# Optimization experiments

Hardware: AMD Instinct MI355X
Metric: run time of the kernel (lower is better)

Reference implementation:

```python
import jax, jax.numpy as jnp
import numpy as np

N = 50000   # nodes per node type
D = 128     # in/out channels
E = 500000  # edges per edge type


def setup_inputs() -> dict:
    key = jax.random.key(0)
    ks = jax.random.split(key, 24)
    s = 1.0 / np.sqrt(D)
    def w(k, shape):
        return jax.random.normal(k, shape, jnp.float32) * s
    inp = {
        "x_a": jax.random.normal(ks[0], (N, D), jnp.float32),
        "x_b": jax.random.normal(ks[1], (N, D), jnp.float32),
        "edge_e1": jax.random.randint(ks[2], (2, E), 0, N),  # a -> b
        "edge_e2": jax.random.randint(ks[3], (2, E), 0, N),  # b -> a
        "edge_e3": jax.random.randint(ks[4], (2, E), 0, N),  # b -> a
    }
    i = 5
    for e in ("e1", "e2", "e3"):
        inp[f"Ws_{e}"] = w(ks[i], (D, D)); i += 1
        inp[f"Wt_{e}"] = w(ks[i], (D, D)); i += 1
        inp[f"wih_{e}"] = w(ks[i], (3 * D, D)); i += 1
        inp[f"whh_{e}"] = w(ks[i], (3 * D, D)); i += 1
        inp[f"bih_{e}"] = jnp.zeros((3 * D,), jnp.float32)
        inp[f"bhh_{e}"] = jnp.zeros((3 * D,), jnp.float32)
    return inp


def _gru_cell(x, h, wih, whh, bih, bhh):
    # PyTorch nn.GRUCell semantics: x = input, h = hidden
    gi = x @ wih.T + bih
    gh = h @ whh.T + bhh
    ir, iz, inn = jnp.split(gi, 3, axis=1)
    hr, hz, hn = jnp.split(gh, 3, axis=1)
    r = jax.nn.sigmoid(ir + hr)
    z = jax.nn.sigmoid(iz + hz)
    n = jnp.tanh(inn + r * hn)
    return (1.0 - z) * n + z * h


def _edge_type(x_src, x_tgt, edge, Ws, Wt, wih, whh, bih, bhh):
    sx = x_src @ Ws.T                       # [Ns, D] per-edge-type source linear (no bias)
    tx = x_tgt @ Wt.T                       # [Nt, D] per-edge-type target linear
    msg = sx[edge[0]]                       # [E, D]  gather by source index
    agg = jax.ops.segment_sum(msg, edge[1], num_segments=x_tgt.shape[0])  # scatter-sum
    return _gru_cell(tx, agg, wih, whh, bih, bhh)


def reference(x_a, x_b, edge_e1, edge_e2, edge_e3,
              Ws_e1, Wt_e1, wih_e1, whh_e1, bih_e1, bhh_e1,
              Ws_e2, Wt_e2, wih_e2, whh_e2, bih_e2, bhh_e2,
              Ws_e3, Wt_e3, wih_e3, whh_e3, bih_e3, bhh_e3):
    # edge type e1: a -> b  (div['b'] = 1)
    out_b = _edge_type(x_a, x_b, edge_e1, Ws_e1, Wt_e1, wih_e1, whh_e1, bih_e1, bhh_e1)
    # edge types e2, e3: b -> a  (div['a'] = 2)
    out_a = _edge_type(x_b, x_a, edge_e2, Ws_e2, Wt_e2, wih_e2, whh_e2, bih_e2, bhh_e2)
    out_a = out_a + _edge_type(x_b, x_a, edge_e3, Ws_e3, Wt_e3, wih_e3, whh_e3, bih_e3, bhh_e3)
    out_a = out_a / 2.0
    out_a = jax.nn.relu(out_a)
    out_b = jax.nn.relu(out_b)
    return jnp.stack([out_a, out_b])  # [2, N, D]
```

## Files before the change

### kernel.cpp

```cpp
#include <hip/hip_runtime.h>
#include <hip/hip_bf16.h>
#include <stdint.h>
#include <math.h>

#define NN 50000
#define DD 128
#define EE 500000
#define ROWT 1563
#define NBIN 98
#define CHB 245

typedef __attribute__((ext_vector_type(8))) short bfx8;
typedef __attribute__((ext_vector_type(4))) short bfx4;
typedef __attribute__((ext_vector_type(4))) float f32x4;
typedef __attribute__((ext_vector_type(4))) int i32x4;
typedef unsigned short u16;

static __device__ __forceinline__ short f2bf(float f) {
  union { float f; uint32_t u; } v; v.f = f;
  uint32_t r = (v.u + 0x7fffu + ((v.u >> 16) & 1u)) >> 16;
  return (short)r;
}
static __device__ __forceinline__ float bf2f(short b) {
  union { uint32_t u; float f; } v; v.u = ((uint32_t)(uint16_t)b) << 16;
  return v.f;
}

static __device__ __forceinline__ void gl_lds16(const short* g, short* l) {
  __builtin_amdgcn_global_load_lds(
      (const __attribute__((address_space(1))) unsigned int*)g,
      (__attribute__((address_space(3))) unsigned int*)l, 16, 0, 0);
}

static __device__ __forceinline__ bfx8 load_pk(const short* p, int ct, int ks, int lane) {
  return *reinterpret_cast<const bfx8*>(p + ((((size_t)ct * 4 + ks) * 64 + lane) << 3));
}

struct PrepArgs {
  const float* csrc[2]; short* cdst[2];
  const float* A[6]; const float* B[6]; short* pout[6];
  const float* psrc[3]; short* pdst[3];
  const int* edge[3]; int* ccnt;
};

__global__ __launch_bounds__(256) void k_prep(PrepArgs p) {
  const int y = blockIdx.y;
  if (y < 2) {
    int i = (blockIdx.x * 256 + threadIdx.x) * 4;
    if (i >= NN * DD) return;
    f32x4 v = *reinterpret_cast<const f32x4*>(p.csrc[y] + i);
    bfx4 o;
    o[0]=f2bf(v[0]); o[1]=f2bf(v[1]); o[2]=f2bf(v[2]); o[3]=f2bf(v[3]);
    *reinterpret_cast<bfx4*>(p.cdst[y] + i) = o;
  } else if (y < 8) {
    if (blockIdx.x >= 192) return;
    const int e = y - 2;
    const float* A = p.A[e];
    const float* B = p.B[e];
    int tid = blockIdx.x * 256 + threadIdx.x;
    int i = tid >> 7, j = tid & 127;
    float acc = 0.f;
    #pragma unroll 4
    for (int k = 0; k < 128; ++k) acc += A[i * 128 + k] * B[k * 128 + j];
    int ct = i >> 4;
    int lane = (i & 15) | ((((j & 31) >> 3)) << 4);
    int ks = j >> 5;
    int elem = j & 7;
    p.pout[e][(((size_t)(ct * 4 + ks) * 64 + lane) << 3) + elem] = f2bf(acc);
  } else if (y < 11) {
    if (blockIdx.x >= 8) return;
    const int jb = y - 8;
    int tid = blockIdx.x * 256 + threadIdx.x;
    int lane = tid & 63, ks = (tid >> 6) & 3, ct = tid >> 8;
    const float* s = p.psrc[jb] + (size_t)(ct * 16 + (lane & 15)) * 128 + ks * 32 + ((lane >> 4) << 3);
    bfx8 o;
    #pragma unroll
    for (int i = 0; i < 8; ++i) o[i] = f2bf(s[i]);
    *reinterpret_cast<bfx8*>(p.pdst[jb] + ((size_t)tid << 3)) = o;
  } else {
    if (blockIdx.x >= CHB) return;
    const int t = y - 11, tid = threadIdx.x;
    __shared__ int cnt[NBIN];
    for (int b = tid; b < NBIN; b += 256) cnt[b] = 0;
    __syncthreads();
    const int* ed = p.edge[t];
    int base = blockIdx.x * 2048;
    #pragma unroll
    for (int m = 0; m < 8; ++m) {
      int i = base + m * 256 + tid;
      if (i < EE) atomicAdd(&cnt[ed[EE + i] >> 9], 1);
    }
    __syncthreads();
    for (int b = tid; b < NBIN; b += 256)
      if (cnt[b]) atomicAdd(&p.ccnt[t * NBIN + b], cnt[b]);
  }
}

struct CsrArgs {
  const int* edge[3];
  int* ccnt;
  int* cstart;
  int* ccur;
  uint32_t* cbkt[3];
  int* offs[3];
  u16* bucket[3];
};

__global__ __launch_bounds__(384) void k_cscan(CsrArgs a) {
  __shared__ int buf[3][128];
  int ty = threadIdx.x >> 7;
  int i = threadIdx.x & 127;
  int v = (i < NBIN) ? a.ccnt[ty * NBIN + i] : 0;
  buf[ty][i] = v;
  __syncthreads();
  for (int off = 1; off < 128; off <<= 1) {
    int tv = (i >= off) ? buf[ty][i - off] : 0;
    __syncthreads();
    buf[ty][i] += tv;
    __syncthreads();
  }
  if (i < NBIN) {
    int excl = buf[ty][i] - v;
    a.cstart[ty * NBIN + i] = excl;
    a.ccur[ty * NBIN + i] = excl;
  }
}

__global__ __launch_bounds__(256) void k_cbin(CsrArgs a) {
  const int t = blockIdx.y, tid = threadIdx.x;
  __shared__ int cnt[NBIN], cur[NBIN];
  for (int b = tid; b < NBIN; b += 256) cnt[b] = 0;
  __syncthreads();
  const int* ed = a.edge[t];
  int base = blockIdx.x * 4096;
  #pragma unroll
  for (int m = 0; m < 16; ++m) {
    int i = base + m * 256 + tid;
    if (i < EE) atomicAdd(&cnt[ed[EE + i] >> 9], 1);
  }
  __syncthreads();
  for (int b = tid; b < NBIN; b += 256)
    cur[b] = cnt[b] ? atomicAdd(&a.ccur[t * NBIN + b], cnt[b]) : 0;
  __syncthreads();
  uint32_t* cb = a.cbkt[t];
  #pragma unroll
  for (int m = 0; m < 16; ++m) {
    int i = base + m * 256 + tid;
    if (i < EE) {
      int tg = ed[EE + i];
      int b = tg >> 9;
      int pos = atomicAdd(&cur[b], 1);
      cb[pos] = (uint32_t)ed[i] | ((uint32_t)(tg & 511) << 20);
    }
  }
}

__global__ __launch_bounds__(256) void k_fsort(CsrArgs a) {
  const int t = blockIdx.y, bin = blockIdx.x, tid = threadIdx.x;
  __shared__ int rc[512], rcur[512], sb[256];
  int s0 = a.cstart[t * NBIN + bin];
  int cntb = a.ccnt[t * NBIN + bin];
  rc[tid] = 0; rc[tid + 256] = 0;
  __syncthreads();
  const uint32_t* cb = a.cbkt[t];
  for (int i = tid; i < cntb; i += 256) atomicAdd(&rc[cb[s0 + i] >> 20], 1);
  __syncthreads();
  int A = rc[2 * tid], B = rc[2 * tid + 1], s = A + B;
  sb[tid] = s;
  __syncthreads();
  for (int off = 1; off < 256; off <<= 1) {
    int v = (tid >= off) ? sb[tid - off] : 0;
    __syncthreads();
    sb[tid] += v;
    __syncthreads();
  }
  int excl = sb[tid] - s;
  rcur[2 * tid] = s0 + excl;
  rcur[2 * tid + 1] = s0 + excl + A;
  int rows0 = bin << 9;
  int nr = NN - rows0; if (nr > 512) nr = 512;
  if (2 * tid < nr)     a.offs[t][rows0 + 2 * tid]     = s0 + excl + A;
  if (2 * tid + 1 < nr) a.offs[t][rows0 + 2 * tid + 1] = s0 + excl + A + B;
  __syncthreads();
  u16* fb = a.bucket[t];
  for (int i = tid; i < cntb; i += 256) {
    uint32_t e = cb[s0 + i];
    int pos = atomicAdd(&rcur[e >> 20], 1);
    fb[pos] = (u16)e;
  }
}

struct GArgs {
  const int* offs[3]; const u16* bkt[3];
  const short* xsrc[3]; short* agg[3];
};

__global__ __launch_bounds__(256) void k_gather(GArgs a) {
  const int ty = blockIdx.y;
  const int* __restrict__ offs = a.offs[ty];
  const u16* __restrict__ bucket = a.bkt[ty];
  const short* __restrict__ xsrc = a.xsrc[ty];
  short* __restrict__ agg = a.agg[ty];
  int tid = threadIdx.x;
  int row = blockIdx.x * 32 + (tid >> 3);
  if (row >= NN) return;
  int c0 = (tid & 7) * 16;
  int start = row ? offs[row - 1] : 0;
  int end = offs[row];
  f32x4 s0 = (f32x4)(0.f), s1 = (f32x4)(0.f), s2 = (f32x4)(0.f), s3 = (f32x4)(0.f);
  int i = start;
  for (; i + 8 <= end; i += 8) {
    const short* pp[8];
    #pragma unroll
    for (int m = 0; m < 8; ++m) pp[m] = xsrc + (size_t)bucket[i + m] * DD + c0;
    #pragma unroll
    for (int m = 0; m < 8; ++m) {
      bfx8 u = *reinterpret_cast<const bfx8*>(pp[m]);
      bfx8 v = *reinterpret_cast<const bfx8*>(pp[m] + 8);
      #pragma unroll
      for (int j = 0; j < 4; ++j) {
        s0[j] += bf2f(u[j]); s1[j] += bf2f(u[4+j]);
        s2[j] += bf2f(v[j]); s3[j] += bf2f(v[4+j]);
      }
    }
  }
  for (; i + 4 <= end; i += 4) {
    const short* pp[4];
    #pragma unroll
    for (int m = 0; m < 4; ++m) pp[m] = xsrc + (size_t)bucket[i + m] * DD + c0;
    #pragma unroll
    for (int m = 0; m < 4; ++m) {
      bfx8 u = *reinterpret_cast<const bfx8*>(pp[m]);
      bfx8 v = *reinterpret_cast<const bfx8*>(pp[m] + 8);
      #pragma unroll
      for (int j = 0; j < 4; ++j) {
        s0[j] += bf2f(u[j]); s1[j] += bf2f(u[4+j]);
        s2[j] += bf2f(v[j]); s3[j] += bf2f(v[4+j]);
      }
    }
  }
  for (; i < end; ++i) {
    const short* p = xsrc + (size_t)bucket[i] * DD + c0;
    bfx8 u = *reinterpret_cast<const bfx8*>(p), v = *reinterpret_cast<const bfx8*>(p + 8);
    #pragma unroll
    for (int j = 0; j < 4; ++j) {
      s0[j] += bf2f(u[j]); s1[j] += bf2f(u[4+j]);
      s2[j] += bf2f(v[j]); s3[j] += bf2f(v[4+j]);
    }
  }
  short* d = agg + (size_t)row * DD + c0;
  bfx8 o0, o1;
  #pragma unroll
  for (int j = 0; j < 4; ++j) {
    o0[j] = f2bf(s0[j]); o0[4+j] = f2bf(s1[j]);
    o1[j] = f2bf(s2[j]); o1[4+j] = f2bf(s3[j]);
  }
  *reinterpret_cast<bfx8*>(d) = o0;
  *reinterpret_cast<bfx8*>(d + 8) = o1;
}

static __device__ __forceinline__ void gru8(const f32x4 h[2], const f32x4 ai[2][3],
                                            const f32x4 ah[2][3],
                                            float bir, float biz, float bin,
                                            float bhr, float bhz, float bhn,
                                            f32x4 res[2]) {
  #pragma unroll
  for (int rf = 0; rf < 2; ++rf)
    #pragma unroll
    for (int q = 0; q < 4; ++q) {
      float ir = ai[rf][0][q] + bir, iz = ai[rf][1][q] + biz, in = ai[rf][2][q] + bin;
      float hr = ah[rf][0][q] + bhr, hz = ah[rf][1][q] + bhz, hn = ah[rf][2][q] + bhn;
      float rr = 1.f / (1.f + __expf(-(ir + hr)));
      float zz = 1.f / (1.f + __expf(-(iz + hz)));
      float t2 = in + rr * hn;
      float nn = 1.f - 2.f / (__expf(2.f * t2) + 1.f);
      res[rf][q] = (1.f - zz) * nn + zz * h[rf][q];
    }
}

static __device__ __forceinline__ void gru_unit(
    const short* lds, int gbase, int ctw, int lane,
    const short* wsp, const short* combp, const short* whhsp,
    f32x4 (&h)[2], f32x4 (&ai)[2][3], f32x4 (&ah)[2][3]) {
  #pragma unroll
  for (int rf = 0; rf < 2; ++rf) {
    h[rf] = (f32x4)(0.f);
    #pragma unroll
    for (int g = 0; g < 3; ++g) { ai[rf][g] = (f32x4)(0.f); ah[rf][g] = (f32x4)(0.f); }
  }
  #pragma unroll
  for (int ks = 0; ks < 4; ++ks) {
    bfx8 x0 = *reinterpret_cast<const bfx8*>(lds + (0 + ks) * 512 + lane * 8);
    bfx8 x1 = *reinterpret_cast<const bfx8*>(lds + (4 + ks) * 512 + lane * 8);
    bfx8 g0 = *reinterpret_cast<const bfx8*>(lds + (gbase + ks) * 512 + lane * 8);
    bfx8 g1 = *reinterpret_cast<const bfx8*>(lds + (gbase + 4 + ks) * 512 + lane * 8);
    bfx8 bws = load_pk(wsp, ctw, ks, lane);
    h[0] = __builtin_amdgcn_mfma_f32_16x16x32_bf16(g0, bws, h[0], 0, 0, 0);
    h[1] = __builtin_amdgcn_mfma_f32_16x16x32_bf16(g1, bws, h[1], 0, 0, 0);
    #pragma unroll
    for (int g = 0; g < 3; ++g) {
      int ct = g * 8 + ctw;
      bfx8 bi = load_pk(combp, ct, ks, lane);
      bfx8 bh = load_pk(whhsp, ct, ks, lane);
      ai[0][g] = __builtin_amdgcn_mfma_f32_16x16x32_bf16(x0, bi, ai[0][g], 0, 0, 0);
      ai[1][g] = __builtin_amdgcn_mfma_f32_16x16x32_bf16(x1, bi, ai[1][g], 0, 0, 0);
      ah[0][g] = __builtin_amdgcn_mfma_f32_16x16x32_bf16(g0, bh, ah[0][g], 0, 0, 0);
      ah[1][g] = __builtin_amdgcn_mfma_f32_16x16x32_bf16(g1, bh, ah[1][g], 0, 0, 0);
    }
  }
}

struct GG1Args {
  const short* aggX; const short* xt;
  const short* wsp; const short* combp; const short* whhsp;
  const float* bih; const float* bhh;
  float* out;
};

__global__ __launch_bounds__(512) void k_ggru1(GG1Args a) {
  __shared__ short lds[16 * 512];
  const int wave = threadIdx.x >> 6, lane = threadIdx.x & 63;
  const int rbase = blockIdx.x * 32;
  const int ctw = wave;

  #pragma unroll
  for (int i = 0; i < 2; ++i) {
    int f = wave * 2 + i;
    const short* src = (f & 8) ? a.aggX : a.xt;
    int r = rbase + ((f >> 2) & 1) * 16 + (lane & 15);
    if (r >= NN) r = NN - 1;
    gl_lds16(src + (size_t)r * DD + (f & 3) * 32 + ((lane >> 4) << 3), lds + f * 512);
  }
  __syncthreads();

  f32x4 h[2], ai[2][3], ah[2][3];
  gru_unit(lds, 8, ctw, lane, a.wsp, a.combp, a.whhsp, h, ai, ah);

  const int col = ctw * 16 + (lane & 15);
  f32x4 res[2];
  gru8(h, ai, ah, a.bih[col], a.bih[128 + col], a.bih[256 + col],
       a.bhh[col], a.bhh[128 + col], a.bhh[256 + col], res);
  const int lq = (lane >> 4) << 2;
  #pragma unroll
  for (int rf = 0; rf < 2; ++rf)
    #pragma unroll
    for (int q = 0; q < 4; ++q) {
      int r = rbase + rf * 16 + lq + q;
      if (r < NN) a.out[(size_t)r * DD + col] = fmaxf(res[rf][q], 0.f);
    }
}

struct GG2Args {
  const short* agg2; const short* agg3; const short* xt;
  const short* wsp2; const short* combp2; const short* whhsp2;
  const short* wsp3; const short* combp3; const short* whhsp3;
  const float* bih2; const float* bhh2;
  const float* bih3; const float* bhh3;
  float* out;
};

__global__ __launch_bounds__(512) void k_ggru2(GG2Args a) {
  __shared__ short lds[24 * 512];
  float* r3buf = (float*)lds;
  const int wave = threadIdx.x >> 6, lane = threadIdx.x & 63;
  const int rbase = (blockIdx.x >> 1) * 32;
  const int colblk = blockIdx.x & 1;
  const int unit = wave >> 2;
  const int ctw = colblk * 4 + (wave & 3);

  #pragma unroll
  for (int i = 0; i < 3; ++i) {
    int f = wave * 3 + i;
    const short* src = (f < 8) ? a.xt : ((f < 16) ? a.agg2 : a.agg3);
    int r = rbase + ((f >> 2) & 1) * 16 + (lane & 15);
    if (r >= NN) r = NN - 1;
    gl_lds16(src + (size_t)r * DD + (f & 3) * 32 + ((lane >> 4) << 3), lds + f * 512);
  }
  __syncthreads();

  const short* wspU   = unit ? a.wsp3   : a.wsp2;
  const short* combpU = unit ? a.combp3 : a.combp2;
  const short* whhspU = unit ? a.whhsp3 : a.whhsp2;
  const float* bihU   = unit ? a.bih3   : a.bih2;
  const float* bhhU   = unit ? a.bhh3   : a.bhh2;
  const int gbase = unit ? 16 : 8;

  f32x4 h[2], ai[2][3], ah[2][3];
  gru_unit(lds, gbase, ctw, lane, wspU, combpU, whhspU, h, ai, ah);

  const int col = ctw * 16 + (lane & 15);
  const int cl = (wave & 3) * 16 + (lane & 15);
  const int lq = (lane >> 4) << 2;
  f32x4 res[2];
  gru8(h, ai, ah, bihU[col], bihU[128 + col], bihU[256 + col],
       bhhU[col], bhhU[128 + col], bhhU[256 + col], res);

  __syncthreads();
  if (unit == 1) {
    #pragma unroll
    for (int rf = 0; rf < 2; ++rf)
      #pragma unroll
      for (int q = 0; q < 4; ++q)
        r3buf[(rf * 16 + lq + q) * 68 + cl] = res[rf][q];
  }
  __syncthreads();
  if (unit == 0) {
    #pragma unroll
    for (int rf = 0; rf < 2; ++rf)
      #pragma unroll
      for (int q = 0; q < 4; ++q) {
        int r = rbase + rf * 16 + lq + q;
        if (r < NN) {
          float r3 = r3buf[(rf * 16 + lq + q) * 68 + cl];
          a.out[(size_t)r * DD + col] = fmaxf((res[rf][q] + r3) * 0.5f, 0.f);
        }
      }
  }
}

extern "C" void kernel_launch(void* const* d_in, const int* in_sizes, int n_in,
                              void* d_out, int out_size, void* d_ws, size_t ws_size,
                              hipStream_t stream) {
  const float* x_a = (const float*)d_in[0];
  const float* x_b = (const float*)d_in[1];
  const int* edges[3] = {(const int*)d_in[2], (const int*)d_in[3], (const int*)d_in[4]};
  const float *Ws[3], *Wt[3], *wih[3], *whh[3], *bih[3], *bhh[3];
  for (int e = 0; e < 3; ++e) {
    int b = 5 + e * 6;
    Ws[e]  = (const float*)d_in[b + 0];
    Wt[e]  = (const float*)d_in[b + 1];
    wih[e] = (const float*)d_in[b + 2];
    whh[e] = (const float*)d_in[b + 3];
    bih[e] = (const float*)d_in[b + 4];
    bhh[e] = (const float*)d_in[b + 5];
  }

  char* ws = (char*)d_ws;
  short* xa_bf  = (short*)ws;
  short* xb_bf  = (short*)(ws + 12800000);
  short* aggX   = (short*)(ws + 25600000);
  int*   offs   = (int*)(ws + 64000000);
  u16*   bucket = (u16*)(ws + 64600000);
  uint32_t* cbkt= (uint32_t*)(ws + 67600000);
  short* pk     = (short*)(ws + 73600000);
  int*   ccnt   = (int*)(ws + 74300000);
  int*   cstart = (int*)(ws + 74310000);
  int*   ccur   = (int*)(ws + 74320000);
  short *wsp[3], *combp[3], *whhsp[3];
  short* aggp[3];
  int* offsp[3]; u16* bktp[3]; uint32_t* cbktp[3];
  for (int e = 0; e < 3; ++e) {
    short* base = pk + (size_t)e * 114688;
    wsp[e] = base; combp[e] = base + 16384; whhsp[e] = base + 65536;
    aggp[e]  = aggX + (size_t)e * NN * DD;
    offsp[e] = offs + (size_t)e * 50000;
    bktp[e]  = bucket + (size_t)e * 500000;
    cbktp[e] = cbkt + (size_t)e * 500000;
  }

  (void)hipMemsetAsync(ccnt, 0, 3 * NBIN * sizeof(int), stream);

  PrepArgs pa;
  pa.csrc[0] = x_a; pa.cdst[0] = xa_bf;
  pa.csrc[1] = x_b; pa.cdst[1] = xb_bf;
  for (int e = 0; e < 3; ++e) {
    pa.A[e] = wih[e];     pa.B[e] = Wt[e]; pa.pout[e] = combp[e];
    pa.A[3 + e] = whh[e]; pa.B[3 + e] = Ws[e]; pa.pout[3 + e] = whhsp[e];
    pa.psrc[e] = Ws[e];   pa.pdst[e] = wsp[e];
    pa.edge[e] = edges[e];
  }
  pa.ccnt = ccnt;
  hipLaunchKernelGGL(k_prep, dim3(6250, 14), dim3(256), 0, stream, pa);

  CsrArgs ca;
  for (int e = 0; e < 3; ++e) {
    ca.edge[e] = edges[e];
    ca.cbkt[e] = cbktp[e];
    ca.offs[e] = offsp[e];
    ca.bucket[e] = bktp[e];
  }
  ca.ccnt = ccnt; ca.cstart = cstart; ca.ccur = ccur;
  hipLaunchKernelGGL(k_cscan, dim3(1), dim3(384), 0, stream, ca);
  hipLaunchKernelGGL(k_cbin, dim3((EE + 4095) / 4096, 3), dim3(256), 0, stream, ca);
  hipLaunchKernelGGL(k_fsort, dim3(NBIN, 3), dim3(256), 0, stream, ca);

  GArgs ga;
  const short* srcb[3] = {xa_bf, xb_bf, xb_bf};
  for (int e = 0; e < 3; ++e) {
    ga.offs[e] = offsp[e]; ga.bkt[e] = bktp[e];
    ga.xsrc[e] = srcb[e];  ga.agg[e] = aggp[e];
  }
  hipLaunchKernelGGL(k_gather, dim3(ROWT, 3), dim3(256), 0, stream, ga);

  float* out_a = (float*)d_out;
  float* out_b = (float*)d_out + (size_t)NN * DD;

  GG1Args g1 = {aggp[0], xb_bf, wsp[0], combp[0], whhsp[0], bih[0], bhh[0], out_b};
  hipLaunchKernelGGL(k_ggru1, dim3(ROWT), dim3(512), 0, stream, g1);

  GG2Args g2 = {aggp[1], aggp[2], xa_bf,
                wsp[1], combp[1], whhsp[1],
                wsp[2], combp[2], whhsp[2],
                bih[1], bhh[1], bih[2], bhh[2], out_a};
  hipLaunchKernelGGL(k_ggru2, dim3(ROWT * 2), dim3(512), 0, stream, g2);
}
```

Before: 228.7 us.

## Fuse CSR gather into GRU kernels, writing aggregates straight to LDS

```diff
diff --git a/kernel.cpp b/kernel.cpp
--- a/kernel.cpp
+++ b/kernel.cpp
@@ -190,73 +190,43 @@
   }
 }
 
-struct GArgs {
-  const int* offs[3]; const u16* bkt[3];
-  const short* xsrc[3]; short* agg[3];
-};
-
-__global__ __launch_bounds__(256) void k_gather(GArgs a) {
-  const int ty = blockIdx.y;
-  const int* __restrict__ offs = a.offs[ty];
-  const u16* __restrict__ bucket = a.bkt[ty];
-  const short* __restrict__ xsrc = a.xsrc[ty];
-  short* __restrict__ agg = a.agg[ty];
-  int tid = threadIdx.x;
-  int row = blockIdx.x * 32 + (tid >> 3);
-  if (row >= NN) return;
-  int c0 = (tid & 7) * 16;
-  int start = row ? offs[row - 1] : 0;
-  int end = offs[row];
-  f32x4 s0 = (f32x4)(0.f), s1 = (f32x4)(0.f), s2 = (f32x4)(0.f), s3 = (f32x4)(0.f);
-  int i = start;
-  for (; i + 8 <= end; i += 8) {
-    const short* pp[8];
-    #pragma unroll
-    for (int m = 0; m < 8; ++m) pp[m] = xsrc + (size_t)bucket[i + m] * DD + c0;
-    #pragma unroll
-    for (int m = 0; m < 8; ++m) {
-      bfx8 u = *reinterpret_cast<const bfx8*>(pp[m]);
-      bfx8 v = *reinterpret_cast<const bfx8*>(pp[m] + 8);
+static __device__ __forceinline__ void gather_slice(
+    const int* __restrict__ offs, const u16* __restrict__ bucket,
+    const short* __restrict__ xsrc, short* lds, int gbase,
+    int rbase, int lr, int c0) {
+  int row = rbase + lr;
+  f32x4 sa = (f32x4)(0.f), sb = (f32x4)(0.f);
+  if (row < NN) {
+    int start = row ? offs[row - 1] : 0;
+    int end = offs[row];
+    int i = start;
+    for (; i + 4 <= end; i += 4) {
+      const short* p0 = xsrc + (size_t)bucket[i]     * DD + c0;
+      const short* p1 = xsrc + (size_t)bucket[i + 1] * DD + c0;
+      const short* p2 = xsrc + (size_t)bucket[i + 2] * DD + c0;
+      const short* p3 = xsrc + (size_t)bucket[i + 3] * DD + c0;
+      bfx8 u0 = *reinterpret_cast<const bfx8*>(p0);
+      bfx8 u1 = *reinterpret_cast<const bfx8*>(p1);
+      bfx8 u2 = *reinterpret_cast<const bfx8*>(p2);
+      bfx8 u3 = *reinterpret_cast<const bfx8*>(p3);
       #pragma unroll
       for (int j = 0; j < 4; ++j) {
-        s0[j] += bf2f(u[j]); s1[j] += bf2f(u[4+j]);
-        s2[j] += bf2f(v[j]); s3[j] += bf2f(v[4+j]);
+        sa[j] += bf2f(u0[j]) + bf2f(u1[j]) + bf2f(u2[j]) + bf2f(u3[j]);
+        sb[j] += bf2f(u0[4+j]) + bf2f(u1[4+j]) + bf2f(u2[4+j]) + bf2f(u3[4+j]);
       }
     }
-  }
-  for (; i + 4 <= end; i += 4) {
-    const short* pp[4];
-    #pragma unroll
-    for (int m = 0; m < 4; ++m) pp[m] = xsrc + (size_t)bucket[i + m] * DD + c0;
-    #pragma unroll
-    for (int m = 0; m < 4; ++m) {
-      bfx8 u = *reinterpret_cast<const bfx8*>(pp[m]);
-      bfx8 v = *reinterpret_cast<const bfx8*>(pp[m] + 8);
+    for (; i < end; ++i) {
+      bfx8 u = *reinterpret_cast<const bfx8*>(xsrc + (size_t)bucket[i] * DD + c0);
       #pragma unroll
-      for (int j = 0; j < 4; ++j) {
-        s0[j] += bf2f(u[j]); s1[j] += bf2f(u[4+j]);
-        s2[j] += bf2f(v[j]); s3[j] += bf2f(v[4+j]);
-      }
-    }
-  }
-  for (; i < end; ++i) {
-    const short* p = xsrc + (size_t)bucket[i] * DD + c0;
-    bfx8 u = *reinterpret_cast<const bfx8*>(p), v = *reinterpret_cast<const bfx8*>(p + 8);
-    #pragma unroll
-    for (int j = 0; j < 4; ++j) {
-      s0[j] += bf2f(u[j]); s1[j] += bf2f(u[4+j]);
-      s2[j] += bf2f(v[j]); s3[j] += bf2f(v[4+j]);
-    }
-  }
-  short* d = agg + (size_t)row * DD + c0;
-  bfx8 o0, o1;
-  #pragma unroll
-  for (int j = 0; j < 4; ++j) {
-    o0[j] = f2bf(s0[j]); o0[4+j] = f2bf(s1[j]);
-    o1[j] = f2bf(s2[j]); o1[4+j] = f2bf(s3[j]);
-  }
-  *reinterpret_cast<bfx8*>(d) = o0;
-  *reinterpret_cast<bfx8*>(d + 8) = o1;
+      for (int j = 0; j < 4; ++j) { sa[j] += bf2f(u[j]); sb[j] += bf2f(u[4+j]); }
+    }
+  }
+  int f = gbase + ((lr >> 4) << 2) + (c0 >> 5);
+  int ln = (lr & 15) | (((c0 & 31) >> 3) << 4);
+  bfx8 o;
+  #pragma unroll
+  for (int j = 0; j < 4; ++j) { o[j] = f2bf(sa[j]); o[4+j] = f2bf(sb[j]); }
+  *reinterpret_cast<bfx8*>(lds + f * 512 + ln * 8) = o;
 }
 
 static __device__ __forceinline__ void gru8(const f32x4 h[2], const f32x4 ai[2][3],
@@ -311,32 +281,34 @@
 }
 
 struct GG1Args {
-  const short* aggX; const short* xt;
+  const short* xgat;
+  const short* xt;
+  const int* offs; const u16* bucket;
   const short* wsp; const short* combp; const short* whhsp;
   const float* bih; const float* bhh;
   float* out;
 };
 
-__global__ __launch_bounds__(512) void k_ggru1(GG1Args a) {
+__global__ __launch_bounds__(512) void k_ggru1f(GG1Args a) {
   __shared__ short lds[16 * 512];
   const int wave = threadIdx.x >> 6, lane = threadIdx.x & 63;
   const int rbase = blockIdx.x * 32;
-  const int ctw = wave;
-
-  #pragma unroll
-  for (int i = 0; i < 2; ++i) {
-    int f = wave * 2 + i;
-    const short* src = (f & 8) ? a.aggX : a.xt;
-    int r = rbase + ((f >> 2) & 1) * 16 + (lane & 15);
+
+  {
+    int r = rbase + ((wave >> 2) & 1) * 16 + (lane & 15);
     if (r >= NN) r = NN - 1;
-    gl_lds16(src + (size_t)r * DD + (f & 3) * 32 + ((lane >> 4) << 3), lds + f * 512);
+    gl_lds16(a.xt + (size_t)r * DD + (wave & 3) * 32 + ((lane >> 4) << 3), lds + wave * 512);
+  }
+  {
+    int t = threadIdx.x;
+    gather_slice(a.offs, a.bucket, a.xgat, lds, 8, rbase, t >> 4, (t & 15) * 8);
   }
   __syncthreads();
 
   f32x4 h[2], ai[2][3], ah[2][3];
-  gru_unit(lds, 8, ctw, lane, a.wsp, a.combp, a.whhsp, h, ai, ah);
-
-  const int col = ctw * 16 + (lane & 15);
+  gru_unit(lds, 8, wave, lane, a.wsp, a.combp, a.whhsp, h, ai, ah);
+
+  const int col = wave * 16 + (lane & 15);
   f32x4 res[2];
   gru8(h, ai, ah, a.bih[col], a.bih[128 + col], a.bih[256 + col],
        a.bhh[col], a.bhh[128 + col], a.bhh[256 + col], res);
@@ -351,7 +323,10 @@
 }
 
 struct GG2Args {
-  const short* agg2; const short* agg3; const short* xt;
+  const short* xgat;
+  const short* xt;
+  const int* offs2; const u16* bucket2;
+  const int* offs3; const u16* bucket3;
   const short* wsp2; const short* combp2; const short* whhsp2;
   const short* wsp3; const short* combp3; const short* whhsp3;
   const float* bih2; const float* bhh2;
@@ -359,22 +334,26 @@
   float* out;
 };
 
-__global__ __launch_bounds__(512) void k_ggru2(GG2Args a) {
+__global__ __launch_bounds__(1024) void k_ggru2f(GG2Args a) {
   __shared__ short lds[24 * 512];
-  float* r3buf = (float*)lds;
+  float* r3buf = (float*)(lds + 8 * 512);
   const int wave = threadIdx.x >> 6, lane = threadIdx.x & 63;
-  const int rbase = (blockIdx.x >> 1) * 32;
-  const int colblk = blockIdx.x & 1;
-  const int unit = wave >> 2;
-  const int ctw = colblk * 4 + (wave & 3);
-
-  #pragma unroll
-  for (int i = 0; i < 3; ++i) {
-    int f = wave * 3 + i;
-    const short* src = (f < 8) ? a.xt : ((f < 16) ? a.agg2 : a.agg3);
-    int r = rbase + ((f >> 2) & 1) * 16 + (lane & 15);
+  const int rbase = blockIdx.x * 32;
+  const int unit = wave >> 3;
+  const int ctw = wave & 7;
+
+  if (unit == 0) {
+    int r = rbase + ((wave >> 2) & 1) * 16 + (lane & 15);
     if (r >= NN) r = NN - 1;
-    gl_lds16(src + (size_t)r * DD + (f & 3) * 32 + ((lane >> 4) << 3), lds + f * 512);
+    gl_lds16(a.xt + (size_t)r * DD + (wave & 3) * 32 + ((lane >> 4) << 3), lds + wave * 512);
+  }
+  {
+    int t = threadIdx.x;
+    int ty = t >> 9;
+    int lr = (t >> 4) & 31;
+    int c0 = (t & 15) * 8;
+    gather_slice(ty ? a.offs3 : a.offs2, ty ? a.bucket3 : a.bucket2,
+                 a.xgat, lds, 8 + ty * 8, rbase, lr, c0);
   }
   __syncthreads();
 
@@ -383,13 +362,11 @@
   const short* whhspU = unit ? a.whhsp3 : a.whhsp2;
   const float* bihU   = unit ? a.bih3   : a.bih2;
   const float* bhhU   = unit ? a.bhh3   : a.bhh2;
-  const int gbase = unit ? 16 : 8;
 
   f32x4 h[2], ai[2][3], ah[2][3];
-  gru_unit(lds, gbase, ctw, lane, wspU, combpU, whhspU, h, ai, ah);
+  gru_unit(lds, unit ? 16 : 8, ctw, lane, wspU, combpU, whhspU, h, ai, ah);
 
   const int col = ctw * 16 + (lane & 15);
-  const int cl = (wave & 3) * 16 + (lane & 15);
   const int lq = (lane >> 4) << 2;
   f32x4 res[2];
   gru8(h, ai, ah, bihU[col], bihU[128 + col], bihU[256 + col],
@@ -401,7 +378,7 @@
     for (int rf = 0; rf < 2; ++rf)
       #pragma unroll
       for (int q = 0; q < 4; ++q)
-        r3buf[(rf * 16 + lq + q) * 68 + cl] = res[rf][q];
+        r3buf[(rf * 16 + lq + q) * 128 + col] = res[rf][q];
   }
   __syncthreads();
   if (unit == 0) {
@@ -411,7 +388,7 @@
       for (int q = 0; q < 4; ++q) {
         int r = rbase + rf * 16 + lq + q;
         if (r < NN) {
-          float r3 = r3buf[(rf * 16 + lq + q) * 68 + cl];
+          float r3 = r3buf[(rf * 16 + lq + q) * 128 + col];
           a.out[(size_t)r * DD + col] = fmaxf((res[rf][q] + r3) * 0.5f, 0.f);
         }
       }
@@ -438,21 +415,18 @@
   char* ws = (char*)d_ws;
   short* xa_bf  = (short*)ws;
   short* xb_bf  = (short*)(ws + 12800000);
-  short* aggX   = (short*)(ws + 25600000);
-  int*   offs   = (int*)(ws + 64000000);
-  u16*   bucket = (u16*)(ws + 64600000);
-  uint32_t* cbkt= (uint32_t*)(ws + 67600000);
-  short* pk     = (short*)(ws + 73600000);
-  int*   ccnt   = (int*)(ws + 74300000);
-  int*   cstart = (int*)(ws + 74310000);
-  int*   ccur   = (int*)(ws + 74320000);
+  int*   offs   = (int*)(ws + 25600000);
+  u16*   bucket = (u16*)(ws + 26200000);
+  uint32_t* cbkt= (uint32_t*)(ws + 29200000);
+  short* pk     = (short*)(ws + 35200000);
+  int*   ccnt   = (int*)(ws + 35900000);
+  int*   cstart = (int*)(ws + 35910000);
+  int*   ccur   = (int*)(ws + 35920000);
   short *wsp[3], *combp[3], *whhsp[3];
-  short* aggp[3];
   int* offsp[3]; u16* bktp[3]; uint32_t* cbktp[3];
   for (int e = 0; e < 3; ++e) {
     short* base = pk + (size_t)e * 114688;
     wsp[e] = base; combp[e] = base + 16384; whhsp[e] = base + 65536;
-    aggp[e]  = aggX + (size_t)e * NN * DD;
     offsp[e] = offs + (size_t)e * 50000;
     bktp[e]  = bucket + (size_t)e * 500000;
     cbktp[e] = cbkt + (size_t)e * 500000;
@@ -484,23 +458,25 @@
   hipLaunchKernelGGL(k_cbin, dim3((EE + 4095) / 4096, 3), dim3(256), 0, stream, ca);
   hipLaunchKernelGGL(k_fsort, dim3(NBIN, 3), dim3(256), 0, stream, ca);
 
-  GArgs ga;
-  const short* srcb[3] = {xa_bf, xb_bf, xb_bf};
-  for (int e = 0; e < 3; ++e) {
-    ga.offs[e] = offsp[e]; ga.bkt[e] = bktp[e];
-    ga.xsrc[e] = srcb[e];  ga.agg[e] = aggp[e];
-  }
-  hipLaunchKernelGGL(k_gather, dim3(ROWT, 3), dim3(256), 0, stream, ga);
-
   float* out_a = (float*)d_out;
   float* out_b = (float*)d_out + (size_t)NN * DD;
 
-  GG1Args g1 = {aggp[0], xb_bf, wsp[0], combp[0], whhsp[0], bih[0], bhh[0], out_b};
-  hipLaunchKernelGGL(k_ggru1, dim3(ROWT), dim3(512), 0, stream, g1);
-
-  GG2Args g2 = {aggp[1], aggp[2], xa_bf,
-                wsp[1], combp[1], whhsp[1],
-                wsp[2], combp[2], whhsp[2],
-                bih[1], bhh[1], bih[2], bhh[2], out_a};
-  hipLaunchKernelGGL(k_ggru2, dim3(ROWT * 2), dim3(512), 0, stream, g2);
-}
+  GG2Args g2;
+  g2.xgat = xb_bf; g2.xt = xa_bf;
+  g2.offs2 = offsp[1]; g2.bucket2 = bktp[1];
+  g2.offs3 = offsp[2]; g2.bucket3 = bktp[2];
+  g2.wsp2 = wsp[1]; g2.combp2 = combp[1]; g2.whhsp2 = whhsp[1];
+  g2.wsp3 = wsp[2]; g2.combp3 = combp[2]; g2.whhsp3 = whhsp[2];
+  g2.bih2 = bih[1]; g2.bhh2 = bhh[1];
+  g2.bih3 = bih[2]; g2.bhh3 = bhh[2];
+  g2.out = out_a;
+  hipLaunchKernelGGL(k_ggru2f, dim3(ROWT), dim3(1024), 0, stream, g2);
+
+  GG1Args g1;
+  g1.xgat = xa_bf; g1.xt = xb_bf;
+  g1.offs = offsp[0]; g1.bucket = bktp[0];
+  g1.wsp = wsp[0]; g1.combp = combp[0]; g1.whhsp = whhsp[0];
+  g1.bih = bih[0]; g1.bhh = bhh[0];
+  g1.out = out_b;
+  hipLaunchKernelGGL(k_ggru1f, dim3(ROWT), dim3(512), 0, stream, g1);
+}
```

Result: slower. 248.4 us (+8.6%).

## Make GRU kernels persistent with double-buffered LDS prefetch

Applied to the files above, without the earlier changes.

```diff
diff --git a/kernel.cpp b/kernel.cpp
--- a/kernel.cpp
+++ b/kernel.cpp
@@ -9,6 +9,8 @@
 #define ROWT 1563
 #define NBIN 98
 #define CHB 245
+#define G2 768
+#define G1 1024
 
 typedef __attribute__((ext_vector_type(8))) short bfx8;
 typedef __attribute__((ext_vector_type(4))) short bfx4;
@@ -270,10 +272,10 @@
     for (int q = 0; q < 4; ++q) {
       float ir = ai[rf][0][q] + bir, iz = ai[rf][1][q] + biz, in = ai[rf][2][q] + bin;
       float hr = ah[rf][0][q] + bhr, hz = ah[rf][1][q] + bhz, hn = ah[rf][2][q] + bhn;
-      float rr = 1.f / (1.f + __expf(-(ir + hr)));
-      float zz = 1.f / (1.f + __expf(-(iz + hz)));
+      float rr = __builtin_amdgcn_rcpf(1.f + __expf(-(ir + hr)));
+      float zz = __builtin_amdgcn_rcpf(1.f + __expf(-(iz + hz)));
       float t2 = in + rr * hn;
-      float nn = 1.f - 2.f / (__expf(2.f * t2) + 1.f);
+      float nn = 1.f - 2.f * __builtin_amdgcn_rcpf(__expf(2.f * t2) + 1.f);
       res[rf][q] = (1.f - zz) * nn + zz * h[rf][q];
     }
 }
@@ -317,37 +319,55 @@
   float* out;
 };
 
-__global__ __launch_bounds__(512) void k_ggru1(GG1Args a) {
-  __shared__ short lds[16 * 512];
-  const int wave = threadIdx.x >> 6, lane = threadIdx.x & 63;
-  const int rbase = blockIdx.x * 32;
-  const int ctw = wave;
-
+static __device__ __forceinline__ void stage1(const GG1Args& a, int vt, short* buf,
+                                              int wave, int lane) {
+  int rbase = vt * 32;
   #pragma unroll
   for (int i = 0; i < 2; ++i) {
     int f = wave * 2 + i;
     const short* src = (f & 8) ? a.aggX : a.xt;
     int r = rbase + ((f >> 2) & 1) * 16 + (lane & 15);
     if (r >= NN) r = NN - 1;
-    gl_lds16(src + (size_t)r * DD + (f & 3) * 32 + ((lane >> 4) << 3), lds + f * 512);
-  }
-  __syncthreads();
-
-  f32x4 h[2], ai[2][3], ah[2][3];
-  gru_unit(lds, 8, ctw, lane, a.wsp, a.combp, a.whhsp, h, ai, ah);
-
-  const int col = ctw * 16 + (lane & 15);
-  f32x4 res[2];
-  gru8(h, ai, ah, a.bih[col], a.bih[128 + col], a.bih[256 + col],
-       a.bhh[col], a.bhh[128 + col], a.bhh[256 + col], res);
+    gl_lds16(src + (size_t)r * DD + (f & 3) * 32 + ((lane >> 4) << 3), buf + f * 512);
+  }
+}
+
+__global__ __launch_bounds__(512) void k_ggru1p(GG1Args a) {
+  __shared__ short lds[2][16 * 512];
+  const int wave = threadIdx.x >> 6, lane = threadIdx.x & 63;
   const int lq = (lane >> 4) << 2;
-  #pragma unroll
-  for (int rf = 0; rf < 2; ++rf)
-    #pragma unroll
-    for (int q = 0; q < 4; ++q) {
-      int r = rbase + rf * 16 + lq + q;
-      if (r < NN) a.out[(size_t)r * DD + col] = fmaxf(res[rf][q], 0.f);
-    }
+  const int col = wave * 16 + (lane & 15);
+  const float bir = a.bih[col], biz = a.bih[128 + col], bin = a.bih[256 + col];
+  const float bhr = a.bhh[col], bhz = a.bhh[128 + col], bhn = a.bhh[256 + col];
+  int cur = 0;
+  stage1(a, blockIdx.x, lds[0], wave, lane);
+  for (int vt = blockIdx.x; vt < ROWT; vt += G1) {
+    int nxt = vt + G1;
+    if (nxt < ROWT) {
+      stage1(a, nxt, lds[cur ^ 1], wave, lane);
+      asm volatile("s_waitcnt vmcnt(2)" ::: "memory");
+    } else {
+      asm volatile("s_waitcnt vmcnt(0)" ::: "memory");
+    }
+    __builtin_amdgcn_s_barrier();
+    __builtin_amdgcn_sched_barrier(0);
+    {
+      int rbase = vt * 32;
+      f32x4 h[2], ai[2][3], ah[2][3];
+      gru_unit(lds[cur], 8, wave, lane, a.wsp, a.combp, a.whhsp, h, ai, ah);
+      f32x4 res[2];
+      gru8(h, ai, ah, bir, biz, bin, bhr, bhz, bhn, res);
+      #pragma unroll
+      for (int rf = 0; rf < 2; ++rf)
+        #pragma unroll
+        for (int q = 0; q < 4; ++q) {
+          int r = rbase + rf * 16 + lq + q;
+          if (r < NN) a.out[(size_t)r * DD + col] = fmaxf(res[rf][q], 0.f);
+        }
+    }
+    __builtin_amdgcn_s_barrier();
+    cur ^= 1;
+  }
 }
 
 struct GG2Args {
@@ -359,62 +379,65 @@
   float* out;
 };
 
-__global__ __launch_bounds__(512) void k_ggru2(GG2Args a) {
-  __shared__ short lds[24 * 512];
-  float* r3buf = (float*)lds;
-  const int wave = threadIdx.x >> 6, lane = threadIdx.x & 63;
-  const int rbase = (blockIdx.x >> 1) * 32;
-  const int colblk = blockIdx.x & 1;
-  const int unit = wave >> 2;
-  const int ctw = colblk * 4 + (wave & 3);
-
+static __device__ __forceinline__ void stage2(const GG2Args& a, int vt, short* buf,
+                                              int wave, int lane) {
+  int rbase = vt * 32;
   #pragma unroll
   for (int i = 0; i < 3; ++i) {
     int f = wave * 3 + i;
     const short* src = (f < 8) ? a.xt : ((f < 16) ? a.agg2 : a.agg3);
     int r = rbase + ((f >> 2) & 1) * 16 + (lane & 15);
     if (r >= NN) r = NN - 1;
-    gl_lds16(src + (size_t)r * DD + (f & 3) * 32 + ((lane >> 4) << 3), lds + f * 512);
-  }
-  __syncthreads();
-
-  const short* wspU   = unit ? a.wsp3   : a.wsp2;
-  const short* combpU = unit ? a.combp3 : a.combp2;
-  const short* whhspU = unit ? a.whhsp3 : a.whhsp2;
-  const float* bihU   = unit ? a.bih3   : a.bih2;
-  const float* bhhU   = unit ? a.bhh3   : a.bhh2;
-  const int gbase = unit ? 16 : 8;
-
-  f32x4 h[2], ai[2][3], ah[2][3];
-  gru_unit(lds, gbase, ctw, lane, wspU, combpU, whhspU, h, ai, ah);
-
-  const int col = ctw * 16 + (lane & 15);
-  const int cl = (wave & 3) * 16 + (lane & 15);
+    gl_lds16(src + (size_t)r * DD + (f & 3) * 32 + ((lane >> 4) << 3), buf + f * 512);
+  }
+}
+
+__global__ __launch_bounds__(512) void k_ggru2p(GG2Args a) {
+  __shared__ short lds[2][24 * 512];
+  const int wave = threadIdx.x >> 6, lane = threadIdx.x & 63;
   const int lq = (lane >> 4) << 2;
-  f32x4 res[2];
-  gru8(h, ai, ah, bihU[col], bihU[128 + col], bihU[256 + col],
-       bhhU[col], bhhU[128 + col], bhhU[256 + col], res);
-
-  __syncthreads();
-  if (unit == 1) {
-    #pragma unroll
-    for (int rf = 0; rf < 2; ++rf)
+  const int col = wave * 16 + (lane & 15);
+  const float b2ir = a.bih2[col], b2iz = a.bih2[128 + col], b2in = a.bih2[256 + col];
+  const float b2hr = a.bhh2[col], b2hz = a.bhh2[128 + col], b2hn = a.bhh2[256 + col];
+  const float b3ir = a.bih3[col], b3iz = a.bih3[128 + col], b3in = a.bih3[256 + col];
+  const float b3hr = a.bhh3[col], b3hz = a.bhh3[128 + col], b3hn = a.bhh3[256 + col];
+  int cur = 0;
+  stage2(a, blockIdx.x, lds[0], wave, lane);
+  for (int vt = blockIdx.x; vt < ROWT; vt += G2) {
+    int nxt = vt + G2;
+    if (nxt < ROWT) {
+      stage2(a, nxt, lds[cur ^ 1], wave, lane);
+      asm volatile("s_waitcnt vmcnt(3)" ::: "memory");
+    } else {
+      asm volatile("s_waitcnt vmcnt(0)" ::: "memory");
+    }
+    __builtin_amdgcn_s_barrier();
+    __builtin_amdgcn_sched_barrier(0);
+    {
+      int rbase = vt * 32;
+      f32x4 res2[2];
+      {
+        f32x4 h[2], ai[2][3], ah[2][3];
+        gru_unit(lds[cur], 8, wave, lane, a.wsp2, a.combp2, a.whhsp2, h, ai, ah);
+        gru8(h, ai, ah, b2ir, b2iz, b2in, b2hr, b2hz, b2hn, res2);
+      }
+      f32x4 res3[2];
+      {
+        f32x4 h[2], ai[2][3], ah[2][3];
+        gru_unit(lds[cur], 16, wave, lane, a.wsp3, a.combp3, a.whhsp3, h, ai, ah);
+        gru8(h, ai, ah, b3ir, b3iz, b3in, b3hr, b3hz, b3hn, res3);
+      }
       #pragma unroll
-      for (int q = 0; q < 4; ++q)
-        r3buf[(rf * 16 + lq + q) * 68 + cl] = res[rf][q];
-  }
-  __syncthreads();
-  if (unit == 0) {
-    #pragma unroll
-    for (int rf = 0; rf < 2; ++rf)
-      #pragma unroll
-      for (int q = 0; q < 4; ++q) {
-        int r = rbase + rf * 16 + lq + q;
-        if (r < NN) {
-          float r3 = r3buf[(rf * 16 + lq + q) * 68 + cl];
-          a.out[(size_t)r * DD + col] = fmaxf((res[rf][q] + r3) * 0.5f, 0.f);
+      for (int rf = 0; rf < 2; ++rf)
+        #pragma unroll
+        for (int q = 0; q < 4; ++q) {
+          int r = rbase + rf * 16 + lq + q;
+          if (r < NN)
+            a.out[(size_t)r * DD + col] = fmaxf((res2[rf][q] + res3[rf][q]) * 0.5f, 0.f);
         }
-      }
+    }
+    __builtin_amdgcn_s_barrier();
+    cur ^= 1;
   }
 }
 
@@ -495,12 +518,12 @@
   float* out_a = (float*)d_out;
   float* out_b = (float*)d_out + (size_t)NN * DD;
 
-  GG1Args g1 = {aggp[0], xb_bf, wsp[0], combp[0], whhsp[0], bih[0], bhh[0], out_b};
-  hipLaunchKernelGGL(k_ggru1, dim3(ROWT), dim3(512), 0, stream, g1);
-
   GG2Args g2 = {aggp[1], aggp[2], xa_bf,
                 wsp[1], combp[1], whhsp[1],
                 wsp[2], combp[2], whhsp[2],
                 bih[1], bhh[1], bih[2], bhh[2], out_a};
-  hipLaunchKernelGGL(k_ggru2, dim3(ROWT * 2), dim3(512), 0, stream, g2);
-}
+  hipLaunchKernelGGL(k_ggru2p, dim3(G2), dim3(512), 0, stream, g2);
+
+  GG1Args g1 = {aggp[0], xb_bf, wsp[0], combp[0], whhsp[0], bih[0], bhh[0], out_b};
+  hipLaunchKernelGGL(k_ggru1p, dim3(G1), dim3(512), 0, stream, g1);
+}
```

Measured after the change: 236.5 us. +3.4%, slower.
